# Performance work log

Measured on AMD Instinct MI355X. Metric: run time of the kernel, lower is better.

The kernel has to match this reference:

```python
import jax, jax.numpy as jnp
import numpy as np

TEMPERATURE = 1.0 / 0.07  # fixed (temperature_trainable=False)
B, D = 256, 65536


def setup_inputs() -> dict:
    key = jax.random.key(0)
    kA, kB = jax.random.split(key)
    feat_A = jax.random.normal(kA, (B, D), dtype=jnp.float32)
    feat_B = jax.random.normal(kB, (B, D), dtype=jnp.float32)
    # L2-normalize (standard for contrastive features; keeps exp(logits) finite)
    feat_A = feat_A / jnp.linalg.norm(feat_A, axis=-1, keepdims=True)
    feat_B = feat_B / jnp.linalg.norm(feat_B, axis=-1, keepdims=True)
    return {"feat_A": feat_A, "feat_B": feat_B}


def reference(feat_A, feat_B):
    # logits[i, j] = <A_i, B_j> * temperature   -- [B, B]
    logits = jnp.einsum("id,jd->ij", feat_A, feat_B) * TEMPERATURE
    pos_logits = jnp.diagonal(logits)  # [B]
    # margin=0.0, dcl=False, index=None -> neg_mask is all True, so
    # log(sum_j exp(logits)) is a full-row/col logsumexp (stable form of exp->sum->log)
    neg_A2B = jax.nn.logsumexp(logits, axis=1)  # A -> B classification
    neg_B2A = jax.nn.logsumexp(logits, axis=0)  # B -> A classification
    loss_A2B = jnp.mean(neg_A2B - pos_logits)
    loss_B2A = jnp.mean(neg_B2A - pos_logits)
    return (loss_A2B + loss_B2A) * 0.5
```

## Files before the change

kernel.cpp:

```cpp
#include <hip/hip_runtime.h>
#include <hip/hip_bf16.h>


#define D_DIM 65536
#define B_DIM 256
#define LDK 72

constexpr float TEMP = 1.0f / 0.07f;

typedef short short8 __attribute__((ext_vector_type(8)));
typedef float floatx4 __attribute__((ext_vector_type(4)));

__device__ inline unsigned short f2bf(float f) {
  unsigned u = __builtin_bit_cast(unsigned, f);
  unsigned rounding = 0x7fffu + ((u >> 16) & 1u);
  return (unsigned short)((u + rounding) >> 16);
}

__device__ inline void st_bf16x4(unsigned short* dst, float4 v) {
  uint2 u;
  u.x = (unsigned)f2bf(v.x) | ((unsigned)f2bf(v.y) << 16);
  u.y = (unsigned)f2bf(v.z) | ((unsigned)f2bf(v.w) << 16);
  *(uint2*)dst = u;
}

__global__ __launch_bounds__(256, 2) void gemm_splitk(
    const float* __restrict__ A, const float* __restrict__ Bm,
    float* __restrict__ partials, int Kc) {
  const int bid = blockIdx.x;
  const int mt = (bid & 1) * 128;
  const int nt = ((bid >> 1) & 1) * 128;
  const int chunk = bid >> 2;
  const size_t k0 = (size_t)chunk * (size_t)Kc;

  __shared__ unsigned short As[128][LDK];
  __shared__ unsigned short Bs[128][LDK];

  const int t = threadIdx.x;
  const int lane = t & 63;
  const int w = t >> 6;
  const int wm = (w & 1) * 64;
  const int wn = (w >> 1) * 64;

  const int lr = t >> 4;
  const int lc = (t & 15) * 4;

  const float* Abase = A + (size_t)(mt + lr) * D_DIM + k0 + lc;
  const float* Bbase = Bm + (size_t)(nt + lr) * D_DIM + k0 + lc;

  floatx4 acc[4][4];
#pragma unroll
  for (int mb = 0; mb < 4; ++mb)
#pragma unroll
    for (int nb = 0; nb < 4; ++nb) acc[mb][nb] = (floatx4)0.f;

  float4 ra[8], rb[8];
  const int nst = Kc >> 6;

#pragma unroll
  for (int p = 0; p < 8; ++p) {
    ra[p] = *(const float4*)(Abase + (size_t)p * 16 * D_DIM);
    rb[p] = *(const float4*)(Bbase + (size_t)p * 16 * D_DIM);
  }

  for (int s = 0; s < nst; ++s) {
#pragma unroll
    for (int p = 0; p < 8; ++p) {
      st_bf16x4(&As[lr + p * 16][lc], ra[p]);
      st_bf16x4(&Bs[lr + p * 16][lc], rb[p]);
    }
    __syncthreads();

    if (s + 1 < nst) {
      const float* Ap = Abase + (size_t)(s + 1) * 64;
      const float* Bp = Bbase + (size_t)(s + 1) * 64;
#pragma unroll
      for (int p = 0; p < 8; ++p) {
        ra[p] = *(const float4*)(Ap + (size_t)p * 16 * D_DIM);
        rb[p] = *(const float4*)(Bp + (size_t)p * 16 * D_DIM);
      }
    }

#pragma unroll
    for (int ks = 0; ks < 64; ks += 32) {
      short8 af[4], bf[4];
      const int ko = ks + (lane >> 4) * 8;
#pragma unroll
      for (int mb = 0; mb < 4; ++mb)
        af[mb] = *(const short8*)&As[wm + mb * 16 + (lane & 15)][ko];
#pragma unroll
      for (int nb = 0; nb < 4; ++nb)
        bf[nb] = *(const short8*)&Bs[wn + nb * 16 + (lane & 15)][ko];
#pragma unroll
      for (int mb = 0; mb < 4; ++mb)
#pragma unroll
        for (int nb = 0; nb < 4; ++nb)
          acc[mb][nb] = __builtin_amdgcn_mfma_f32_16x16x32_bf16(
              af[mb], bf[nb], acc[mb][nb], 0, 0, 0);
    }
    __syncthreads();
  }

  float* outp = partials + (size_t)chunk * (B_DIM * B_DIM);
#pragma unroll
  for (int mb = 0; mb < 4; ++mb) {
#pragma unroll
    for (int nb = 0; nb < 4; ++nb) {
      const int gi0 = mt + wm + mb * 16 + ((lane >> 4) * 4);
      const int gj = nt + wn + nb * 16 + (lane & 15);
#pragma unroll
      for (int r = 0; r < 4; ++r)
        outp[(size_t)(gi0 + r) * B_DIM + gj] = acc[mb][nb][r];
    }
  }
}

__global__ void finalize_rows(const float* __restrict__ partials,
                              float* __restrict__ logits,
                              float* __restrict__ rowout, int C) {
  const int i = blockIdx.x;
  const int j = threadIdx.x;
  const float* p = partials + (size_t)i * B_DIM + j;
  float s = 0.f;
#pragma unroll 32
  for (int c = 0; c < C; ++c) s += p[(size_t)c * (B_DIM * B_DIM)];
  const float lg = s * TEMP;
  logits[i * B_DIM + j] = lg;

  __shared__ float posv;
  if (j == i) posv = lg;

  float e = expf(lg);
#pragma unroll
  for (int off = 32; off > 0; off >>= 1) e += __shfl_down(e, off);
  __shared__ float wsum[4];
  if ((j & 63) == 0) wsum[j >> 6] = e;
  __syncthreads();
  if (j == 0) {
    const float tot = wsum[0] + wsum[1] + wsum[2] + wsum[3];
    rowout[i] = logf(tot) - 2.f * posv;
  }
}

__global__ void finalize_cols(const float* __restrict__ logits,
                              float* __restrict__ colout) {
  const int j = blockIdx.x;
  const int i = threadIdx.x;
  float e = expf(logits[(size_t)i * B_DIM + j]);
#pragma unroll
  for (int off = 32; off > 0; off >>= 1) e += __shfl_down(e, off);
  __shared__ float wsum[4];
  if ((i & 63) == 0) wsum[i >> 6] = e;
  __syncthreads();
  if (i == 0) {
    const float tot = wsum[0] + wsum[1] + wsum[2] + wsum[3];
    colout[j] = logf(tot);
  }
}

__global__ void finalize_out(const float* __restrict__ rowout,
                             const float* __restrict__ colout,
                             float* __restrict__ out) {
  const int t = threadIdx.x;
  float v = rowout[t] + colout[t];
#pragma unroll
  for (int off = 32; off > 0; off >>= 1) v += __shfl_down(v, off);
  __shared__ float wsum[4];
  if ((t & 63) == 0) wsum[t >> 6] = v;
  __syncthreads();
  if (t == 0) out[0] = (wsum[0] + wsum[1] + wsum[2] + wsum[3]) * (0.5f / 256.f);
}

extern "C" void kernel_launch(void* const* d_in, const int* in_sizes, int n_in,
                              void* d_out, int out_size, void* d_ws, size_t ws_size,
                              hipStream_t stream) {
  (void)in_sizes; (void)n_in; (void)out_size;
  const float* A = (const float*)d_in[0];
  const float* Bm = (const float*)d_in[1];
  float* out = (float*)d_out;

  const size_t per = (size_t)B_DIM * B_DIM * sizeof(float);
  int C = 128;
  while (C > 1 && (size_t)(C + 1) * per + 2 * B_DIM * sizeof(float) > ws_size)
    C >>= 1;
  const int Kc = D_DIM / C;

  float* logits = (float*)d_ws;
  float* partials = (float*)d_ws + (size_t)B_DIM * B_DIM;
  float* rowout = partials + (size_t)C * B_DIM * B_DIM;
  float* colout = rowout + B_DIM;

  gemm_splitk<<<4 * C, 256, 0, stream>>>(A, Bm, partials, Kc);
  finalize_rows<<<B_DIM, B_DIM, 0, stream>>>(partials, logits, rowout, C);
  finalize_cols<<<B_DIM, B_DIM, 0, stream>>>(logits, colout);
  finalize_out<<<1, B_DIM, 0, stream>>>(rowout, colout, out);
}
```

Before: 163.7 us.

## Double-buffer LDS tiles and prefetch two stages ahead in split-K GEMM

```diff
diff --git a/kernel.cpp b/kernel.cpp
--- a/kernel.cpp
+++ b/kernel.cpp
@@ -33,8 +33,8 @@
   const int chunk = bid >> 2;
   const size_t k0 = (size_t)chunk * (size_t)Kc;
 
-  __shared__ unsigned short As[128][LDK];
-  __shared__ unsigned short Bs[128][LDK];
+  __shared__ unsigned short As[2][128][LDK];
+  __shared__ unsigned short Bs[2][128][LDK];
 
   const int t = threadIdx.x;
   const int lane = t & 63;
@@ -54,51 +54,60 @@
 #pragma unroll
     for (int nb = 0; nb < 4; ++nb) acc[mb][nb] = (floatx4)0.f;
 
-  float4 ra[8], rb[8];
+  float4 raE[8], rbE[8], raO[8], rbO[8];
   const int nst = Kc >> 6;
 
-#pragma unroll
-  for (int p = 0; p < 8; ++p) {
-    ra[p] = *(const float4*)(Abase + (size_t)p * 16 * D_DIM);
-    rb[p] = *(const float4*)(Bbase + (size_t)p * 16 * D_DIM);
-  }
-
-  for (int s = 0; s < nst; ++s) {
-#pragma unroll
-    for (int p = 0; p < 8; ++p) {
-      st_bf16x4(&As[lr + p * 16][lc], ra[p]);
-      st_bf16x4(&Bs[lr + p * 16][lc], rb[p]);
-    }
-    __syncthreads();
-
-    if (s + 1 < nst) {
-      const float* Ap = Abase + (size_t)(s + 1) * 64;
-      const float* Bp = Bbase + (size_t)(s + 1) * 64;
-#pragma unroll
-      for (int p = 0; p < 8; ++p) {
-        ra[p] = *(const float4*)(Ap + (size_t)p * 16 * D_DIM);
-        rb[p] = *(const float4*)(Bp + (size_t)p * 16 * D_DIM);
-      }
-    }
-
-#pragma unroll
-    for (int ks = 0; ks < 64; ks += 32) {
-      short8 af[4], bf[4];
-      const int ko = ks + (lane >> 4) * 8;
-#pragma unroll
-      for (int mb = 0; mb < 4; ++mb)
-        af[mb] = *(const short8*)&As[wm + mb * 16 + (lane & 15)][ko];
-#pragma unroll
-      for (int nb = 0; nb < 4; ++nb)
-        bf[nb] = *(const short8*)&Bs[wn + nb * 16 + (lane & 15)][ko];
-#pragma unroll
-      for (int mb = 0; mb < 4; ++mb)
-#pragma unroll
-        for (int nb = 0; nb < 4; ++nb)
-          acc[mb][nb] = __builtin_amdgcn_mfma_f32_16x16x32_bf16(
-              af[mb], bf[nb], acc[mb][nb], 0, 0, 0);
-    }
-    __syncthreads();
+#define LOADSET(ra, rb, S)                                                 \
+  {                                                                        \
+    const float* Ap_ = Abase + (size_t)(S)*64;                             \
+    const float* Bp_ = Bbase + (size_t)(S)*64;                             \
+    _Pragma("unroll") for (int p = 0; p < 8; ++p) {                        \
+      ra[p] = *(const float4*)(Ap_ + (size_t)p * 16 * D_DIM);              \
+      rb[p] = *(const float4*)(Bp_ + (size_t)p * 16 * D_DIM);              \
+    }                                                                      \
+  }
+
+#define STAGE(ra, rb, BUF)                                                 \
+  {                                                                        \
+    _Pragma("unroll") for (int p = 0; p < 8; ++p) {                        \
+      st_bf16x4(&As[BUF][lr + p * 16][lc], ra[p]);                         \
+      st_bf16x4(&Bs[BUF][lr + p * 16][lc], rb[p]);                         \
+    }                                                                      \
+  }
+
+#define MFMA_BUF(BUF)                                                      \
+  {                                                                        \
+    _Pragma("unroll") for (int ks = 0; ks < 64; ks += 32) {                \
+      short8 af[4], bf[4];                                                 \
+      const int ko = ks + (lane >> 4) * 8;                                 \
+      _Pragma("unroll") for (int mb = 0; mb < 4; ++mb)                     \
+          af[mb] = *(const short8*)&As[BUF][wm + mb * 16 + (lane & 15)][ko]; \
+      _Pragma("unroll") for (int nb = 0; nb < 4; ++nb)                     \
+          bf[nb] = *(const short8*)&Bs[BUF][wn + nb * 16 + (lane & 15)][ko]; \
+      _Pragma("unroll") for (int mb = 0; mb < 4; ++mb)                     \
+          _Pragma("unroll") for (int nb = 0; nb < 4; ++nb)                 \
+              acc[mb][nb] = __builtin_amdgcn_mfma_f32_16x16x32_bf16(       \
+                  af[mb], bf[nb], acc[mb][nb], 0, 0, 0);                   \
+    }                                                                      \
+  }
+
+  LOADSET(raE, rbE, 0)
+  LOADSET(raO, rbO, 1)
+
+  for (int s = 0; s < nst; s += 2) {
+    STAGE(raE, rbE, 0)
+    asm volatile("s_waitcnt lgkmcnt(0)" ::: "memory");
+    __builtin_amdgcn_s_barrier();
+    __builtin_amdgcn_sched_barrier(0);
+    if (s + 2 < nst) LOADSET(raE, rbE, s + 2)
+    MFMA_BUF(0)
+
+    STAGE(raO, rbO, 1)
+    asm volatile("s_waitcnt lgkmcnt(0)" ::: "memory");
+    __builtin_amdgcn_s_barrier();
+    __builtin_amdgcn_sched_barrier(0);
+    if (s + 3 < nst) LOADSET(raO, rbO, s + 3)
+    MFMA_BUF(1)
   }
 
   float* outp = partials + (size_t)chunk * (B_DIM * B_DIM);
```

Result: no change. 162.4 us (-0.8%).
